# Kernel tuning notes

Measured on AMD Instinct MI355X. Metric: run time of the kernel, lower is better.

Reference implementation:

```python
import jax, jax.numpy as jnp
import numpy as np

EPS = 1e-6
TAU = 0.07


def setup_inputs() -> dict:
    key = jax.random.key(0)
    kx, ky = jax.random.split(key)
    B, D = 4096, 1024
    x = jax.random.normal(kx, (B, D), dtype=jnp.float32)
    y = jax.random.normal(ky, (B, D), dtype=jnp.float32)
    return {"x": x, "y": y}


def reference(x, y):
    B = x.shape[0]
    # torch CosineSimilarity: dot / (max(||x||, eps) * max(||y||, eps))
    xn = x / jnp.maximum(jnp.linalg.norm(x, axis=-1, keepdims=True), EPS)
    yn = y / jnp.maximum(jnp.linalg.norm(y, axis=-1, keepdims=True), EPS)
    S = jnp.einsum('id,jd->ij', xn, yn)          # [B, B] cosine sims, S[i,j]=cos(x_i,y_j)
    E = jnp.exp(S / TAU)                          # bounded: |S|<=1 so exp <= e^{1/0.07}
    diag = jnp.diagonal(E)
    # original: sum_j (exp + eps) + eps  ->  sum_j exp + B*eps + eps
    extra = B * EPS + EPS
    row_denom = jnp.sum(E, axis=1) + extra        # x->y direction (loop 1)
    col_denom = jnp.sum(E, axis=0) + extra        # y->x direction (loop 2)
    coef = -1.0 / (2.0 * B)
    loss = coef * (jnp.sum(jnp.log(diag / row_denom)) + jnp.sum(jnp.log(diag / col_denom)))
    return loss
```

## Files before the change

### kernel.cpp

```cpp
#include <hip/hip_runtime.h>

#define NB 4096
#define DK 1024
#define EPSF 1e-6f
#define QS 32.0f

typedef __attribute__((ext_vector_type(8))) int   i32x8_t;
typedef __attribute__((ext_vector_type(4))) int   i32x4_t;
typedef __attribute__((ext_vector_type(4))) float f32x4_t;

#if defined(__has_builtin)
#if __has_builtin(__builtin_amdgcn_cvt_scalef32_pk_fp4_f32)
#define HW_FP4 1
#endif
#endif


__device__ __forceinline__ void async16(const void* g, void* lds) {
    __builtin_amdgcn_global_load_lds(
        (const __attribute__((address_space(1))) void*)g,
        (__attribute__((address_space(3))) void*)lds, 16, 0, 0);
}

__device__ __forceinline__ unsigned enc4(float v) {
    const float a = fabsf(v);
    unsigned c = (a >= 0.25f) + (a >= 0.75f) + (a >= 1.25f) + (a >= 1.75f)
               + (a >= 2.5f)  + (a >= 3.5f)  + (a >= 5.0f);
    return c | ((v < 0.f) ? 8u : 0u);
}

__global__ __launch_bounds__(256) void normalize_rows(
    const float* __restrict__ x, const float* __restrict__ y,
    unsigned char* __restrict__ xq, unsigned char* __restrict__ yq,
    float* __restrict__ sdiag, float* __restrict__ zerobuf)
{
    const int t = threadIdx.x;
    const int gid = blockIdx.x * 256 + t;
    if (gid < 2 * NB) zerobuf[gid] = 0.f;
    if (gid == 0) *((unsigned*)(zerobuf + 3 * NB)) = 0u;

    const int wave = t >> 6;
    const int lane = t & 63;
    const int row  = blockIdx.x * 4 + wave;

    const float4* xr = reinterpret_cast<const float4*>(x + (size_t)row * DK);
    const float4* yr = reinterpret_cast<const float4*>(y + (size_t)row * DK);

    float4 xv[4], yv[4];
    float ssx = 0.f, ssy = 0.f, sxy = 0.f;
    #pragma unroll
    for (int jj = 0; jj < 4; ++jj) {
        xv[jj] = xr[lane * 4 + jj];
        yv[jj] = yr[lane * 4 + jj];
        ssx += xv[jj].x*xv[jj].x + xv[jj].y*xv[jj].y + xv[jj].z*xv[jj].z + xv[jj].w*xv[jj].w;
        ssy += yv[jj].x*yv[jj].x + yv[jj].y*yv[jj].y + yv[jj].z*yv[jj].z + yv[jj].w*yv[jj].w;
        sxy += xv[jj].x*yv[jj].x + xv[jj].y*yv[jj].y + xv[jj].z*yv[jj].z + xv[jj].w*yv[jj].w;
    }
    #pragma unroll
    for (int off = 1; off < 64; off <<= 1) {
        ssx += __shfl_xor(ssx, off, 64);
        ssy += __shfl_xor(ssy, off, 64);
        sxy += __shfl_xor(sxy, off, 64);
    }
    const float invx = 1.0f / fmaxf(sqrtf(ssx), EPSF);
    const float invy = 1.0f / fmaxf(sqrtf(ssy), EPSF);
    const float sx = invx * QS;
    const float sy = invy * QS;

    float fx[16], fy[16];
    #pragma unroll
    for (int jj = 0; jj < 4; ++jj) {
        fx[jj*4+0] = xv[jj].x; fx[jj*4+1] = xv[jj].y;
        fx[jj*4+2] = xv[jj].z; fx[jj*4+3] = xv[jj].w;
        fy[jj*4+0] = yv[jj].x; fy[jj*4+1] = yv[jj].y;
        fy[jj*4+2] = yv[jj].z; fy[jj*4+3] = yv[jj].w;
    }

    unsigned xb0, xb1, yb0, yb1;
#ifdef HW_FP4
    #define CVT8(dst, f, s)                                                        \
        dst = __builtin_amdgcn_cvt_scalef32_pk_fp4_f32(0u,  (f)[0]*(s), (f)[1]*(s), 1.0f, 0); \
        dst = __builtin_amdgcn_cvt_scalef32_pk_fp4_f32(dst, (f)[2]*(s), (f)[3]*(s), 1.0f, 1); \
        dst = __builtin_amdgcn_cvt_scalef32_pk_fp4_f32(dst, (f)[4]*(s), (f)[5]*(s), 1.0f, 2); \
        dst = __builtin_amdgcn_cvt_scalef32_pk_fp4_f32(dst, (f)[6]*(s), (f)[7]*(s), 1.0f, 3)
    CVT8(xb0, fx,     sx);
    CVT8(xb1, fx + 8, sx);
    CVT8(yb0, fy,     sy);
    CVT8(yb1, fy + 8, sy);
    #undef CVT8
#else
    unsigned xb[2] = {0u, 0u}, yb[2] = {0u, 0u};
    #pragma unroll
    for (int j = 0; j < 16; ++j) {
        xb[j >> 3] |= enc4(fx[j] * sx) << ((j & 7) * 4);
        yb[j >> 3] |= enc4(fy[j] * sy) << ((j & 7) * 4);
    }
    xb0 = xb[0]; xb1 = xb[1]; yb0 = yb[0]; yb1 = yb[1];
#endif

    const int p = row >> 4, r = row & 15;
    const unsigned off = (unsigned)p * 8192 + (lane >> 3) * 1024 + r * 64
                       + ((((lane & 7) >> 1) ^ (r & 3)) << 4) + (lane & 1) * 8;
    *reinterpret_cast<uint2*>(xq + off) = make_uint2(xb0, xb1);
    *reinterpret_cast<uint2*>(yq + off) = make_uint2(yb0, yb1);

    if (lane == 0) sdiag[row] = sxy * invx * invy;
}

__global__ __launch_bounds__(512, 4) void gemm_exp_sums(
    const unsigned char* __restrict__ xq, const unsigned char* __restrict__ yq,
    float* __restrict__ rowsum, float* __restrict__ colsum,
    const float* __restrict__ sdiag, unsigned* __restrict__ donecnt,
    float* __restrict__ out)
{
    __shared__ __align__(16) unsigned char LDS[3][24576];
    __shared__ unsigned lastFlag;
    __shared__ double dred[8];

    const int t    = threadIdx.x;
    const int lane = t & 63;
    const int wave = t >> 6;
    const int q    = lane >> 4;
    const int l15  = lane & 15;

    const int R0 = blockIdx.y * 128;
    const int C0 = blockIdx.x * 256;
    const int wRow = (wave >> 2) * 64;
    const int wCol = (wave & 3) * 64;

    f32x4_t acc[4][4];
    #pragma unroll
    for (int i = 0; i < 4; i++)
        #pragma unroll
        for (int j = 0; j < 4; j++)
            acc[i][j] = (f32x4_t){0.f, 0.f, 0.f, 0.f};

    const unsigned char* srcA =
        xq + (size_t)((R0 >> 4) + wave) * 8192 + lane * 16;
    const unsigned char* srcB =
        yq + (size_t)((C0 >> 4) + 2 * wave) * 8192 + lane * 16;

    const int sl = (q ^ (l15 & 3)) << 4;

    auto issue = [&](int kb, int buf) {
        async16(srcA + kb * 1024, &LDS[buf][wave * 1024]);
        #pragma unroll
        for (int pp = 0; pp < 2; ++pp)
            async16(srcB + pp * 8192 + kb * 1024,
                    &LDS[buf][8192 + (2 * wave + pp) * 1024]);
    };

    issue(0, 0);
    issue(1, 1);

    #pragma unroll 1
    for (int kb = 0; kb < 8; ++kb) {
        const int buf = kb % 3;
        if (kb < 6) {
            issue(kb + 2, (kb + 2) % 3);
            __builtin_amdgcn_s_waitcnt(0xF76);
        } else if (kb == 6) {
            __builtin_amdgcn_s_waitcnt(0xF73);
        } else {
            __builtin_amdgcn_s_waitcnt(0xF70);
        }
        __builtin_amdgcn_s_barrier();

        #pragma unroll
        for (int nth = 0; nth < 2; ++nth) {
            i32x8_t bfr[2];
            #pragma unroll
            for (int ni = 0; ni < 2; ++ni) {
                const i32x4_t v = *reinterpret_cast<const i32x4_t*>(
                    &LDS[buf][8192 + ((wCol >> 4) + nth * 2 + ni) * 1024 + l15 * 64 + sl]);
                bfr[ni][0] = v[0]; bfr[ni][1] = v[1]; bfr[ni][2] = v[2]; bfr[ni][3] = v[3];
                bfr[ni][4] = 0;    bfr[ni][5] = 0;    bfr[ni][6] = 0;    bfr[ni][7] = 0;
            }
            #pragma unroll
            for (int mt = 0; mt < 4; ++mt) {
                const i32x4_t v = *reinterpret_cast<const i32x4_t*>(
                    &LDS[buf][((wRow >> 4) + mt) * 1024 + l15 * 64 + sl]);
                i32x8_t af;
                af[0] = v[0]; af[1] = v[1]; af[2] = v[2]; af[3] = v[3];
                af[4] = 0;    af[5] = 0;    af[6] = 0;    af[7] = 0;
                #pragma unroll
                for (int ni = 0; ni < 2; ++ni)
                    acc[mt][nth * 2 + ni] = __builtin_amdgcn_mfma_scale_f32_16x16x128_f8f6f4(
                        af, bfr[ni], acc[mt][nth * 2 + ni],
                        4, 4,
                        0, 0x7F7F7F7F,
                        0, 0x7F7F7F7F);
            }
        }

        __builtin_amdgcn_s_barrier();
    }

    const float kScale = (float)(1.0 / (1024.0 * 0.07 * 0.6931471805599453));
    float csum[4] = {0.f, 0.f, 0.f, 0.f};
    #pragma unroll
    for (int mt = 0; mt < 4; ++mt) {
        float rsum[4] = {0.f, 0.f, 0.f, 0.f};
        #pragma unroll
        for (int nt = 0; nt < 4; ++nt) {
            #pragma unroll
            for (int r = 0; r < 4; ++r) {
                const float e = exp2f(acc[mt][nt][r] * kScale);
                rsum[r]  += e;
                csum[nt] += e;
            }
        }
        #pragma unroll
        for (int r = 0; r < 4; ++r) {
            float v = rsum[r];
            v += __shfl_xor(v, 1, 64);
            v += __shfl_xor(v, 2, 64);
            v += __shfl_xor(v, 4, 64);
            v += __shfl_xor(v, 8, 64);
            if (l15 == 0)
                atomicAdd(&rowsum[R0 + wRow + mt * 16 + q * 4 + r], v);
        }
    }
    #pragma unroll
    for (int nt = 0; nt < 4; ++nt) {
        float v = csum[nt];
        v += __shfl_xor(v, 16, 64);
        v += __shfl_xor(v, 32, 64);
        if (lane < 16)
            atomicAdd(&colsum[C0 + wCol + nt * 16 + l15], v);
    }

    __syncthreads();
    if (t == 0) {
        __threadfence();
        const unsigned old = __hip_atomic_fetch_add(
            donecnt, 1u, __ATOMIC_ACQ_REL, __HIP_MEMORY_SCOPE_AGENT);
        lastFlag = (old == 511u) ? 1u : 0u;
    }
    __syncthreads();
    if (lastFlag) {
        const float extra = (float)(NB * 1e-6 + 1e-6);
        double local = 0.0;
        for (int i = t; i < NB; i += 512) {
            const float rs = __hip_atomic_load(&rowsum[i], __ATOMIC_RELAXED,
                                               __HIP_MEMORY_SCOPE_AGENT);
            const float cs = __hip_atomic_load(&colsum[i], __ATOMIC_RELAXED,
                                               __HIP_MEMORY_SCOPE_AGENT);
            local += (double)sdiag[i] * (2.0 / 0.07)
                   - (double)logf(rs + extra)
                   - (double)logf(cs + extra);
        }
        #pragma unroll
        for (int off = 1; off < 64; off <<= 1)
            local += __shfl_xor(local, off, 64);
        if ((t & 63) == 0) dred[t >> 6] = local;
        __syncthreads();
        if (t == 0) {
            double tot = 0.0;
            #pragma unroll
            for (int w = 0; w < 8; ++w) tot += dred[w];
            out[0] = (float)(tot * (-1.0 / (2.0 * NB)));
        }
    }
}

extern "C" void kernel_launch(void* const* d_in, const int* in_sizes, int n_in,
                              void* d_out, int out_size, void* d_ws, size_t ws_size,
                              hipStream_t stream)
{
    const float* x = (const float*)d_in[0];
    const float* y = (const float*)d_in[1];
    float* out = (float*)d_out;

    char* ws = (char*)d_ws;
    unsigned char* xq = (unsigned char*)ws;
    unsigned char* yq = (unsigned char*)(ws + (size_t)2 * 1024 * 1024);
    float* rowsum = (float*)(ws + (size_t)8 * 1024 * 1024);
    float* colsum = rowsum + NB;
    float* sdiag  = colsum + NB;
    unsigned* donecnt = (unsigned*)(sdiag + NB);

    normalize_rows<<<NB / 4, 256, 0, stream>>>(x, y, xq, yq, sdiag, rowsum);

    dim3 grid(16, 32);
    gemm_exp_sums<<<grid, 512, 0, stream>>>(xq, yq, rowsum, colsum,
                                            sdiag, donecnt, out);
}
```

Before: 105.7 us.

## Load FP4 MFMA operands directly from global, drop LDS pipeline, add finalize kernel

The GEMM kernel no longer stages A/B tiles through a triple-buffered LDS pipeline with async global-to-LDS loads and barriers. Each wave now loads its MFMA fragments straight from global memory in a linear, unswizzled packed layout, which removes the barriers and the LDS traffic. The last-block done-counter reduction is replaced by a separate single-block finalize kernel. In exchange, operand reuse across waves moves from LDS to L2/L1, adds a kernel launch, and halves the occupancy hint.

```diff
diff --git a/kernel.cpp b/kernel.cpp
--- a/kernel.cpp
+++ b/kernel.cpp
@@ -16,12 +16,6 @@
 #endif
 
 
-__device__ __forceinline__ void async16(const void* g, void* lds) {
-    __builtin_amdgcn_global_load_lds(
-        (const __attribute__((address_space(1))) void*)g,
-        (__attribute__((address_space(3))) void*)lds, 16, 0, 0);
-}
-
 __device__ __forceinline__ unsigned enc4(float v) {
     const float a = fabsf(v);
     unsigned c = (a >= 0.25f) + (a >= 0.75f) + (a >= 1.25f) + (a >= 1.75f)
@@ -37,7 +31,6 @@
     const int t = threadIdx.x;
     const int gid = blockIdx.x * 256 + t;
     if (gid < 2 * NB) zerobuf[gid] = 0.f;
-    if (gid == 0) *((unsigned*)(zerobuf + 3 * NB)) = 0u;
 
     const int wave = t >> 6;
     const int lane = t & 63;
@@ -100,23 +93,17 @@
 
     const int p = row >> 4, r = row & 15;
     const unsigned off = (unsigned)p * 8192 + (lane >> 3) * 1024 + r * 64
-                       + ((((lane & 7) >> 1) ^ (r & 3)) << 4) + (lane & 1) * 8;
+                       + (lane & 7) * 8;
     *reinterpret_cast<uint2*>(xq + off) = make_uint2(xb0, xb1);
     *reinterpret_cast<uint2*>(yq + off) = make_uint2(yb0, yb1);
 
     if (lane == 0) sdiag[row] = sxy * invx * invy;
 }
 
-__global__ __launch_bounds__(512, 4) void gemm_exp_sums(
+__global__ __launch_bounds__(512, 2) void gemm_exp_sums(
     const unsigned char* __restrict__ xq, const unsigned char* __restrict__ yq,
-    float* __restrict__ rowsum, float* __restrict__ colsum,
-    const float* __restrict__ sdiag, unsigned* __restrict__ donecnt,
-    float* __restrict__ out)
-{
-    __shared__ __align__(16) unsigned char LDS[3][24576];
-    __shared__ unsigned lastFlag;
-    __shared__ double dred[8];
-
+    float* __restrict__ rowsum, float* __restrict__ colsum)
+{
     const int t    = threadIdx.x;
     const int lane = t & 63;
     const int wave = t >> 6;
@@ -135,65 +122,30 @@
         for (int j = 0; j < 4; j++)
             acc[i][j] = (f32x4_t){0.f, 0.f, 0.f, 0.f};
 
-    const unsigned char* srcA =
-        xq + (size_t)((R0 >> 4) + wave) * 8192 + lane * 16;
-    const unsigned char* srcB =
-        yq + (size_t)((C0 >> 4) + 2 * wave) * 8192 + lane * 16;
-
-    const int sl = (q ^ (l15 & 3)) << 4;
-
-    auto issue = [&](int kb, int buf) {
-        async16(srcA + kb * 1024, &LDS[buf][wave * 1024]);
-        #pragma unroll
-        for (int pp = 0; pp < 2; ++pp)
-            async16(srcB + pp * 8192 + kb * 1024,
-                    &LDS[buf][8192 + (2 * wave + pp) * 1024]);
-    };
-
-    issue(0, 0);
-    issue(1, 1);
-
-    #pragma unroll 1
+    const unsigned char* pA = xq + (size_t)((R0 + wRow) >> 4) * 8192 + l15 * 64 + q * 16;
+    const unsigned char* pB = yq + (size_t)((C0 + wCol) >> 4) * 8192 + l15 * 64 + q * 16;
+
+    #pragma unroll
     for (int kb = 0; kb < 8; ++kb) {
-        const int buf = kb % 3;
-        if (kb < 6) {
-            issue(kb + 2, (kb + 2) % 3);
-            __builtin_amdgcn_s_waitcnt(0xF76);
-        } else if (kb == 6) {
-            __builtin_amdgcn_s_waitcnt(0xF73);
-        } else {
-            __builtin_amdgcn_s_waitcnt(0xF70);
-        }
-        __builtin_amdgcn_s_barrier();
-
-        #pragma unroll
-        for (int nth = 0; nth < 2; ++nth) {
-            i32x8_t bfr[2];
+        i32x4_t a4[4], b4[4];
+        #pragma unroll
+        for (int i = 0; i < 4; ++i) {
+            a4[i] = *reinterpret_cast<const i32x4_t*>(pA + (size_t)i * 8192 + kb * 1024);
+            b4[i] = *reinterpret_cast<const i32x4_t*>(pB + (size_t)i * 8192 + kb * 1024);
+        }
+        #pragma unroll
+        for (int mt = 0; mt < 4; ++mt) {
+            const i32x8_t af = {a4[mt][0], a4[mt][1], a4[mt][2], a4[mt][3], 0, 0, 0, 0};
             #pragma unroll
-            for (int ni = 0; ni < 2; ++ni) {
-                const i32x4_t v = *reinterpret_cast<const i32x4_t*>(
-                    &LDS[buf][8192 + ((wCol >> 4) + nth * 2 + ni) * 1024 + l15 * 64 + sl]);
-                bfr[ni][0] = v[0]; bfr[ni][1] = v[1]; bfr[ni][2] = v[2]; bfr[ni][3] = v[3];
-                bfr[ni][4] = 0;    bfr[ni][5] = 0;    bfr[ni][6] = 0;    bfr[ni][7] = 0;
+            for (int nt = 0; nt < 4; ++nt) {
+                const i32x8_t bf = {b4[nt][0], b4[nt][1], b4[nt][2], b4[nt][3], 0, 0, 0, 0};
+                acc[mt][nt] = __builtin_amdgcn_mfma_scale_f32_16x16x128_f8f6f4(
+                    af, bf, acc[mt][nt],
+                    4, 4,
+                    0, 0x7F7F7F7F,
+                    0, 0x7F7F7F7F);
             }
-            #pragma unroll
-            for (int mt = 0; mt < 4; ++mt) {
-                const i32x4_t v = *reinterpret_cast<const i32x4_t*>(
-                    &LDS[buf][((wRow >> 4) + mt) * 1024 + l15 * 64 + sl]);
-                i32x8_t af;
-                af[0] = v[0]; af[1] = v[1]; af[2] = v[2]; af[3] = v[3];
-                af[4] = 0;    af[5] = 0;    af[6] = 0;    af[7] = 0;
-                #pragma unroll
-                for (int ni = 0; ni < 2; ++ni)
-                    acc[mt][nth * 2 + ni] = __builtin_amdgcn_mfma_scale_f32_16x16x128_f8f6f4(
-                        af, bfr[ni], acc[mt][nth * 2 + ni],
-                        4, 4,
-                        0, 0x7F7F7F7F,
-                        0, 0x7F7F7F7F);
-            }
-        }
-
-        __builtin_amdgcn_s_barrier();
+        }
     }
 
     const float kScale = (float)(1.0 / (1024.0 * 0.07 * 0.6931471805599453));
@@ -229,38 +181,31 @@
         if (lane < 16)
             atomicAdd(&colsum[C0 + wCol + nt * 16 + l15], v);
     }
-
+}
+
+__global__ __launch_bounds__(1024) void finalize(
+    const float* __restrict__ rowsum, const float* __restrict__ colsum,
+    const float* __restrict__ sdiag, float* __restrict__ out)
+{
+    const float extra = (float)(NB * 1e-6 + 1e-6);
+    double local = 0.0;
+    for (int i = threadIdx.x; i < NB; i += 1024) {
+        local += (double)sdiag[i] * (2.0 / 0.07)
+               - (double)logf(rowsum[i] + extra)
+               - (double)logf(colsum[i] + extra);
+    }
+    #pragma unroll
+    for (int off = 1; off < 64; off <<= 1)
+        local += __shfl_xor(local, off, 64);
+    __shared__ double dred[16];
+    const int wave = threadIdx.x >> 6;
+    if ((threadIdx.x & 63) == 0) dred[wave] = local;
     __syncthreads();
-    if (t == 0) {
-        __threadfence();
-        const unsigned old = __hip_atomic_fetch_add(
-            donecnt, 1u, __ATOMIC_ACQ_REL, __HIP_MEMORY_SCOPE_AGENT);
-        lastFlag = (old == 511u) ? 1u : 0u;
-    }
-    __syncthreads();
-    if (lastFlag) {
-        const float extra = (float)(NB * 1e-6 + 1e-6);
-        double local = 0.0;
-        for (int i = t; i < NB; i += 512) {
-            const float rs = __hip_atomic_load(&rowsum[i], __ATOMIC_RELAXED,
-                                               __HIP_MEMORY_SCOPE_AGENT);
-            const float cs = __hip_atomic_load(&colsum[i], __ATOMIC_RELAXED,
-                                               __HIP_MEMORY_SCOPE_AGENT);
-            local += (double)sdiag[i] * (2.0 / 0.07)
-                   - (double)logf(rs + extra)
-                   - (double)logf(cs + extra);
-        }
-        #pragma unroll
-        for (int off = 1; off < 64; off <<= 1)
-            local += __shfl_xor(local, off, 64);
-        if ((t & 63) == 0) dred[t >> 6] = local;
-        __syncthreads();
-        if (t == 0) {
-            double tot = 0.0;
-            #pragma unroll
-            for (int w = 0; w < 8; ++w) tot += dred[w];
-            out[0] = (float)(tot * (-1.0 / (2.0 * NB)));
-        }
+    if (threadIdx.x == 0) {
+        double tot = 0.0;
+        #pragma unroll
+        for (int w = 0; w < 16; ++w) tot += dred[w];
+        out[0] = (float)(tot * (-1.0 / (2.0 * NB)));
     }
 }
 
@@ -278,11 +223,11 @@
     float* rowsum = (float*)(ws + (size_t)8 * 1024 * 1024);
     float* colsum = rowsum + NB;
     float* sdiag  = colsum + NB;
-    unsigned* donecnt = (unsigned*)(sdiag + NB);
 
     normalize_rows<<<NB / 4, 256, 0, stream>>>(x, y, xq, yq, sdiag, rowsum);
 
     dim3 grid(16, 32);
-    gemm_exp_sums<<<grid, 512, 0, stream>>>(xq, yq, rowsum, colsum,
-                                            sdiag, donecnt, out);
-}
+    gemm_exp_sums<<<grid, 512, 0, stream>>>(xq, yq, rowsum, colsum);
+
+    finalize<<<1, 1024, 0, stream>>>(rowsum, colsum, sdiag, out);
+}
```

Result: slower. 116.9 us (+10.6%).
